# Optimization experiments

Measured on AMD Instinct MI355X. Metric: run time of the kernel, lower is better.

## Reference

```python
import jax, jax.numpy as jnp
from jax import lax
import numpy as np

B, T, U, V = 8, 256, 101, 512  # batch, max frames, max labels + 1, vocab (blank = 0)
BLANK = 0
NEG = -1e30  # finite -inf substitute (grad-safe in logaddexp)


def setup_inputs() -> dict:
    key = jax.random.key(0)
    k1, k2 = jax.random.split(key)
    acts = jax.random.normal(k1, (B, T, U, V), dtype=jnp.float32)
    labels = jax.random.randint(k2, (B, U - 1), 1, V).astype(jnp.int32)  # avoid blank idx
    act_lens = jnp.full((B,), T, dtype=jnp.int32)
    label_lens = jnp.full((B,), U - 1, dtype=jnp.int32)
    return {"acts": acts, "labels": labels, "act_lens": act_lens, "label_lens": label_lens}


def _rnnt_per_example(blankp, emit, tlen, ulen):
    # blankp: (T, U) log P(blank | t, u); emit: (T, U-1) log P(label_u | t, u)
    # alpha[0, u] = cumsum_u emit[0, :u]
    row0 = jnp.concatenate([jnp.zeros((1,), blankp.dtype), jnp.cumsum(emit[0])])

    # per-row recurrence: alpha[t, u] = logaddexp(alpha[t-1, u] + blank[t-1, u],
    #                                             alpha[t, u-1] + emit[t, u-1])
    # linear log-space recurrence x_u = logaddexp(b_u, x_{u-1} + a_u) -> associative scan
    def combine(l, r):
        aL, bL = l
        aR, bR = r
        return aL + aR, jnp.logaddexp(bR, bL + aR)

    def step(prev_row, xs):
        blank_tm1, emit_t = xs
        b = prev_row + blank_tm1                              # vertical (blank) transition
        a = jnp.concatenate([jnp.full((1,), NEG, blankp.dtype), emit_t])  # horizontal (emit)
        _, x = lax.associative_scan(combine, (a, b))
        return x, x

    _, rows = lax.scan(step, row0, (blankp[:-1], emit[1:]))
    alpha = jnp.concatenate([row0[None, :], rows], axis=0)    # (T, U)
    # loss = -log P(y|x) = -(alpha[T-1, U_label] + log P(blank | T-1, U_label))
    return -(alpha[tlen - 1, ulen] + blankp[tlen - 1, ulen])


def rnnt_loss(acts, labels, act_lens, label_lens):
    logp = jax.nn.log_softmax(acts, axis=-1)                  # (B, T, U, V)
    blankp = logp[..., BLANK]                                 # (B, T, U)
    lab = jnp.broadcast_to(
        labels[:, None, :, None].astype(jnp.int32),
        (acts.shape[0], acts.shape[1], labels.shape[1], 1),
    )
    emit = jnp.take_along_axis(logp[:, :, :-1, :], lab, axis=3)[..., 0]  # (B, T, U-1)
    return jax.vmap(_rnnt_per_example)(blankp, emit, act_lens, label_lens)


def reference(acts, labels, act_lens, label_lens):
    # reduction='none': per-example RNNT negative log-likelihood, shape (B,)
    return rnnt_loss(acts, labels, act_lens, label_lens)
```

## Files before the change

### kernel.cpp

```cpp
#include <hip/hip_runtime.h>

#define B_ 8
#define T_ 256
#define U_ 101
#define V_ 512
#define UM1 (U_ - 1)
#define DSTR 128
#define DALLOC 488
#define CH 32
#define NCH 12
#define CS 512.0f
#define LOG2E 1.4426950408889634f
#define LN2 0.6931471805599453f

typedef float floatx4 __attribute__((ext_vector_type(4)));
typedef float floatx2 __attribute__((ext_vector_type(2)));

__device__ __forceinline__ float wave_shr1_zero(float x) {
  int r = __builtin_amdgcn_update_dpp(0, __float_as_int(x), 0x138, 0xF, 0xF,
                                      false);
  return __int_as_float(r);
}

__global__ __launch_bounds__(256) void lse_kernel(
    const float* __restrict__ acts, const int* __restrict__ labels,
    const int* __restrict__ act_lens, const int* __restrict__ label_lens,
    float* __restrict__ blankD, float* __restrict__ emitD,
    float* __restrict__ bp2) {
  const int wv = blockIdx.x * 4 + (threadIdx.x >> 6);
  const int lane = threadIdx.x & 63;
  const int r0 = wv * 2;
  const int r1 = r0 + 1;
  const floatx4* p0 = (const floatx4*)(acts + (size_t)r0 * V_);
  const floatx4* p1 = (const floatx4*)(acts + (size_t)r1 * V_);
  floatx4 a0 = p0[lane];
  floatx4 a1 = p0[lane + 64];
  floatx4 c0 = p1[lane];
  floatx4 c1 = p1[lane + 64];
  float s0 = __builtin_exp2f(a0.x * LOG2E) + __builtin_exp2f(a0.y * LOG2E) +
             __builtin_exp2f(a0.z * LOG2E) + __builtin_exp2f(a0.w * LOG2E) +
             __builtin_exp2f(a1.x * LOG2E) + __builtin_exp2f(a1.y * LOG2E) +
             __builtin_exp2f(a1.z * LOG2E) + __builtin_exp2f(a1.w * LOG2E);
  float s1 = __builtin_exp2f(c0.x * LOG2E) + __builtin_exp2f(c0.y * LOG2E) +
             __builtin_exp2f(c0.z * LOG2E) + __builtin_exp2f(c0.w * LOG2E) +
             __builtin_exp2f(c1.x * LOG2E) + __builtin_exp2f(c1.y * LOG2E) +
             __builtin_exp2f(c1.z * LOG2E) + __builtin_exp2f(c1.w * LOG2E);
#pragma unroll
  for (int s = 32; s >= 1; s >>= 1) {
    s0 += __shfl_xor(s0, s);
    s1 += __shfl_xor(s1, s);
  }

#define EMIT_ROW(r, v0, v1, ssum)                                             \
  {                                                                           \
    const int u = (r) % U_;                                                   \
    const int bt = (r) / U_;                                                  \
    const int t = bt % T_;                                                    \
    const int b = bt / T_;                                                    \
    float emitv = 0.0f;                                                       \
    if (u < UM1) {                                                            \
      int e = labels[b * UM1 + u];                             \
      floatx4 sel = (e < 256) ? v0 : v1;                                      \
      int k = e & 3;                                                          \
      float cand =                                                            \
          (k == 0) ? sel.x : (k == 1) ? sel.y : (k == 2) ? sel.z : sel.w;     \
      emitv = __shfl(cand, (e & 255) >> 2);                                   \
    }                                                                         \
    if (lane == 0) {                                                          \
      const float rs = CS * __builtin_amdgcn_rcpf(ssum);                      \
      blankD[((size_t)b * DALLOC + (t + u + 1)) * DSTR + u] =                 \
          __builtin_exp2f(v0.x * LOG2E) * rs;                                 \
      if (u < UM1)                                                            \
        emitD[((size_t)b * DALLOC + (t + u + 1)) * DSTR + (u + 1)] =          \
            __builtin_exp2f(emitv * LOG2E) * rs;                              \
      if (t == act_lens[b] - 1 && u == label_lens[b])                         \
        bp2[b] = v0.x * LOG2E - __builtin_log2f(ssum);                        \
    }                                                                         \
  }

  EMIT_ROW(r0, a0, a1, s0)
  EMIT_ROW(r1, c0, c1, s1)
#undef EMIT_ROW
}

__global__ __launch_bounds__(64, 1) void dp_kernel(
    const float* __restrict__ blankD, const float* __restrict__ emitD,
    const float* __restrict__ bp2, const int* __restrict__ act_lens,
    const int* __restrict__ label_lens, float* __restrict__ out) {
  __shared__ float lds[2][2][CH][DSTR];
  const int b = blockIdx.x;
  const int lane = threadIdx.x;
  const int tl1 = act_lens[b] - 1;
  const int ulen = label_lens[b];
  const int dtar = tl1 + ulen;
  const bool capE = ((ulen & 1) == 0) && (lane == (ulen >> 1));
  const bool capO = ((ulen & 1) == 1) && (lane == (ulen >> 1));
  const floatx4* g4B = (const floatx4*)(blankD + (size_t)b * DALLOC * DSTR);
  const floatx4* g4E = (const floatx4*)(emitD + (size_t)b * DALLOC * DSTR);

  floatx4 rB[16], rE[16];
#pragma unroll
  for (int j = 0; j < 16; ++j) {
    rB[j] = g4B[32 + j * 64 + lane];
    rE[j] = g4E[32 + j * 64 + lane];
  }
  {
    floatx4* lB4 = (floatx4*)&lds[0][0][0][0];
    floatx4* lE4 = (floatx4*)&lds[0][1][0][0];
#pragma unroll
    for (int j = 0; j < 16; ++j) {
      lB4[j * 64 + lane] = rB[j];
      lE4[j * 64 + lane] = rE[j];
    }
  }
  float xE = (lane == 0) ? 1.0f : 0.0f;
  float xO = 0.0f;
  float res = 0.0f, capS = 0.0f, S = 0.0f;

  for (int c = 0; c < NCH; ++c) {
    const int buf = c & 1;
    const int nb = ((c + 1) * CH + 1) * 32;
#pragma unroll
    for (int j = 0; j < 16; ++j) {
      rB[j] = g4B[(size_t)nb + j * 64 + lane];
      rE[j] = g4E[(size_t)nb + j * 64 + lane];
    }
    const floatx2* lB2 = (const floatx2*)&lds[buf][0][0][0];
    const floatx2* lE2 = (const floatx2*)&lds[buf][1][0][0];
    floatx2 pB[8], pE[8];
#pragma unroll
    for (int k = 0; k < 8; ++k) {
      pB[k] = lB2[k * 64 + lane];
      pE[k] = lE2[k * 64 + lane];
    }
    const int dbase = c * CH + 1;
#pragma unroll
    for (int k = 0; k < CH; ++k) {
      const int d = dbase + k;
      const floatx2 Bv = pB[k & 7];
      const floatx2 Ev = pE[k & 7];
      if (k + 8 < CH) {
        pB[k & 7] = lB2[(k + 8) * 64 + lane];
        pE[k & 7] = lE2[(k + 8) * 64 + lane];
      }
      const float xm1E = wave_shr1_zero(xO);
      const float nxE = __builtin_fmaf(xE, Bv.x, xm1E * Ev.x);
      const float nxO = __builtin_fmaf(xO, Bv.y, xE * Ev.y);
      if (d == dtar) {
        res = capE ? nxE : (capO ? nxO : res);
        capS = S;
      }
      xE = nxE;
      xO = nxO;
    }
    float m = fmaxf(xE, xO);
#pragma unroll
    for (int s = 32; s >= 1; s >>= 1) m = fmaxf(m, __shfl_xor(m, s));
    if (m > 0.0f) {
      const float ex = floorf(__builtin_log2f(m));
      const float sc = __builtin_exp2f(-ex);
      xE *= sc;
      xO *= sc;
      S += ex;
    }
    floatx4* wB4 = (floatx4*)&lds[buf ^ 1][0][0][0];
    floatx4* wE4 = (floatx4*)&lds[buf ^ 1][1][0][0];
#pragma unroll
    for (int j = 0; j < 16; ++j) {
      wB4[j * 64 + lane] = rB[j];
      wE4[j * 64 + lane] = rE[j];
    }
  }
  if (capE || capO)
    out[b] = -((__builtin_log2f(res) + capS - 9.0f * (float)dtar + bp2[b]) *
               LN2);
}

extern "C" void kernel_launch(void* const* d_in, const int* in_sizes, int n_in,
                              void* d_out, int out_size, void* d_ws, size_t ws_size,
                              hipStream_t stream) {
  const float* acts = (const float*)d_in[0];
  const int* labels = (const int*)d_in[1];
  const int* act_lens = (const int*)d_in[2];
  const int* label_lens = (const int*)d_in[3];
  float* out = (float*)d_out;
  float* blankD = (float*)d_ws;
  float* emitD = blankD + (size_t)B_ * DALLOC * DSTR;
  float* bp2 = emitD + (size_t)B_ * DALLOC * DSTR;
  hipMemsetAsync(blankD, 0, (size_t)2 * B_ * DALLOC * DSTR * sizeof(float),
                 stream);
  const int nwaves2 = B_ * T_ * U_ / 2;
  lse_kernel<<<nwaves2 / 4, 256, 0, stream>>>(acts, labels, act_lens,
                                              label_lens, blankD, emitD, bp2);
  dp_kernel<<<B_, 64, 0, stream>>>(blankD, emitD, bp2, act_lens, label_lens,
                                   out);
}
```

Measured before the change: 103.6 us.

## Split RNNT DP into forward and backward halves meeting at mid-diagonal

The serial anti-diagonal recurrence per batch is split into a forward pass from the start and a backward (beta) pass from the end, each covering about half the diagonals on separate workgroups (16 blocks instead of 8). A small combine kernel takes the dot product of the two state vectors at the meeting diagonal to get the total probability. This halves the serial dependency chain of the latency-bound DP. In exchange it adds a kernel launch and relies on the backward transitions and scaling bookkeeping being correct for general lengths.

Result: faster. 95.57 us (-7.7%).

```diff
diff --git a/kernel.cpp b/kernel.cpp
--- a/kernel.cpp
+++ b/kernel.cpp
@@ -8,7 +8,7 @@
 #define DSTR 128
 #define DALLOC 488
 #define CH 32
-#define NCH 12
+#define NCHD 6
 #define CS 512.0f
 #define LOG2E 1.4426950408889634f
 #define LN2 0.6931471805599453f
@@ -21,12 +21,15 @@
                                       false);
   return __int_as_float(r);
 }
+__device__ __forceinline__ float wave_shl1_zero(float x) {
+  int r = __builtin_amdgcn_update_dpp(0, __float_as_int(x), 0x130, 0xF, 0xF,
+                                      false);
+  return __int_as_float(r);
+}
 
 __global__ __launch_bounds__(256) void lse_kernel(
     const float* __restrict__ acts, const int* __restrict__ labels,
-    const int* __restrict__ act_lens, const int* __restrict__ label_lens,
-    float* __restrict__ blankD, float* __restrict__ emitD,
-    float* __restrict__ bp2) {
+    float* __restrict__ blankD, float* __restrict__ emitD) {
   const int wv = blockIdx.x * 4 + (threadIdx.x >> 6);
   const int lane = threadIdx.x & 63;
   const int r0 = wv * 2;
@@ -73,8 +76,6 @@
       if (u < UM1)                                                            \
         emitD[((size_t)b * DALLOC + (t + u + 1)) * DSTR + (u + 1)] =          \
             __builtin_exp2f(emitv * LOG2E) * rs;                              \
-      if (t == act_lens[b] - 1 && u == label_lens[b])                         \
-        bp2[b] = v0.x * LOG2E - __builtin_log2f(ssum);                        \
     }                                                                         \
   }
 
@@ -85,95 +86,188 @@
 
 __global__ __launch_bounds__(64, 1) void dp_kernel(
     const float* __restrict__ blankD, const float* __restrict__ emitD,
-    const float* __restrict__ bp2, const int* __restrict__ act_lens,
-    const int* __restrict__ label_lens, float* __restrict__ out) {
+    const int* __restrict__ act_lens, const int* __restrict__ label_lens,
+    float* __restrict__ stateA, float* __restrict__ stateB) {
   __shared__ float lds[2][2][CH][DSTR];
-  const int b = blockIdx.x;
+  const int bid = blockIdx.x;
+  const int b = bid & 7;
+  const bool fwd = (bid < 8);
   const int lane = threadIdx.x;
   const int tl1 = act_lens[b] - 1;
   const int ulen = label_lens[b];
   const int dtar = tl1 + ulen;
-  const bool capE = ((ulen & 1) == 0) && (lane == (ulen >> 1));
-  const bool capO = ((ulen & 1) == 1) && (lane == (ulen >> 1));
+  const int dmid = dtar >> 1;
   const floatx4* g4B = (const floatx4*)(blankD + (size_t)b * DALLOC * DSTR);
   const floatx4* g4E = (const floatx4*)(emitD + (size_t)b * DALLOC * DSTR);
-
   floatx4 rB[16], rE[16];
-#pragma unroll
-  for (int j = 0; j < 16; ++j) {
-    rB[j] = g4B[32 + j * 64 + lane];
-    rE[j] = g4E[32 + j * 64 + lane];
-  }
-  {
-    floatx4* lB4 = (floatx4*)&lds[0][0][0][0];
-    floatx4* lE4 = (floatx4*)&lds[0][1][0][0];
+  float xE, xO, S = 0.0f;
+
+  if (fwd) {
 #pragma unroll
     for (int j = 0; j < 16; ++j) {
-      lB4[j * 64 + lane] = rB[j];
-      lE4[j * 64 + lane] = rE[j];
-    }
-  }
-  float xE = (lane == 0) ? 1.0f : 0.0f;
-  float xO = 0.0f;
-  float res = 0.0f, capS = 0.0f, S = 0.0f;
-
-  for (int c = 0; c < NCH; ++c) {
-    const int buf = c & 1;
-    const int nb = ((c + 1) * CH + 1) * 32;
+      rB[j] = g4B[32 + j * 64 + lane];
+      rE[j] = g4E[32 + j * 64 + lane];
+    }
+    {
+      floatx4* lB4 = (floatx4*)&lds[0][0][0][0];
+      floatx4* lE4 = (floatx4*)&lds[0][1][0][0];
+#pragma unroll
+      for (int j = 0; j < 16; ++j) {
+        lB4[j * 64 + lane] = rB[j];
+        lE4[j * 64 + lane] = rE[j];
+      }
+    }
+    xE = (lane == 0) ? 1.0f : 0.0f;
+    xO = 0.0f;
+    for (int c = 0; c < NCHD; ++c) {
+      const int buf = c & 1;
+      const int nb = ((c + 1) * CH + 1) * 32;
+#pragma unroll
+      for (int j = 0; j < 16; ++j) {
+        rB[j] = g4B[(size_t)nb + j * 64 + lane];
+        rE[j] = g4E[(size_t)nb + j * 64 + lane];
+      }
+      const floatx2* lB2 = (const floatx2*)&lds[buf][0][0][0];
+      const floatx2* lE2 = (const floatx2*)&lds[buf][1][0][0];
+      floatx2 pB[8], pE[8];
+#pragma unroll
+      for (int k = 0; k < 8; ++k) {
+        pB[k] = lB2[k * 64 + lane];
+        pE[k] = lE2[k * 64 + lane];
+      }
+      const int dbase = c * CH + 1;
+#pragma unroll
+      for (int k = 0; k < CH; ++k) {
+        const int d = dbase + k;
+        const floatx2 Bv = pB[k & 7];
+        const floatx2 Ev = pE[k & 7];
+        if (k + 8 < CH) {
+          pB[k & 7] = lB2[(k + 8) * 64 + lane];
+          pE[k & 7] = lE2[(k + 8) * 64 + lane];
+        }
+        const float xm1E = wave_shr1_zero(xO);
+        const float nxE = __builtin_fmaf(xE, Bv.x, xm1E * Ev.x);
+        const float nxO = __builtin_fmaf(xO, Bv.y, xE * Ev.y);
+        const bool go = (d <= dmid);
+        xE = go ? nxE : xE;
+        xO = go ? nxO : xO;
+      }
+      float m = fmaxf(xE, xO);
+#pragma unroll
+      for (int s = 32; s >= 1; s >>= 1) m = fmaxf(m, __shfl_xor(m, s));
+      if (m > 0.0f) {
+        const float ex = floorf(__builtin_log2f(m));
+        const float sc = __builtin_exp2f(-ex);
+        xE *= sc;
+        xO *= sc;
+        S += ex;
+      }
+      floatx4* wB4 = (floatx4*)&lds[buf ^ 1][0][0][0];
+      floatx4* wE4 = (floatx4*)&lds[buf ^ 1][1][0][0];
+#pragma unroll
+      for (int j = 0; j < 16; ++j) {
+        wB4[j * 64 + lane] = rB[j];
+        wE4[j * 64 + lane] = rE[j];
+      }
+    }
+    float* sA = stateA + b * 132;
+    ((floatx2*)sA)[lane] = floatx2{xE, xO};
+    if (lane == 0) sA[128] = S;
+  } else {
+    const int R00 = dtar - 31;
 #pragma unroll
     for (int j = 0; j < 16; ++j) {
-      rB[j] = g4B[(size_t)nb + j * 64 + lane];
-      rE[j] = g4E[(size_t)nb + j * 64 + lane];
-    }
-    const floatx2* lB2 = (const floatx2*)&lds[buf][0][0][0];
-    const floatx2* lE2 = (const floatx2*)&lds[buf][1][0][0];
-    floatx2 pB[8], pE[8];
-#pragma unroll
-    for (int k = 0; k < 8; ++k) {
-      pB[k] = lB2[k * 64 + lane];
-      pE[k] = lE2[k * 64 + lane];
-    }
-    const int dbase = c * CH + 1;
-#pragma unroll
-    for (int k = 0; k < CH; ++k) {
-      const int d = dbase + k;
-      const floatx2 Bv = pB[k & 7];
-      const floatx2 Ev = pE[k & 7];
-      if (k + 8 < CH) {
-        pB[k & 7] = lB2[(k + 8) * 64 + lane];
-        pE[k & 7] = lE2[(k + 8) * 64 + lane];
-      }
-      const float xm1E = wave_shr1_zero(xO);
-      const float nxE = __builtin_fmaf(xE, Bv.x, xm1E * Ev.x);
-      const float nxO = __builtin_fmaf(xO, Bv.y, xE * Ev.y);
-      if (d == dtar) {
-        res = capE ? nxE : (capO ? nxO : res);
-        capS = S;
-      }
-      xE = nxE;
-      xO = nxO;
-    }
-    float m = fmaxf(xE, xO);
-#pragma unroll
-    for (int s = 32; s >= 1; s >>= 1) m = fmaxf(m, __shfl_xor(m, s));
-    if (m > 0.0f) {
-      const float ex = floorf(__builtin_log2f(m));
-      const float sc = __builtin_exp2f(-ex);
-      xE *= sc;
-      xO *= sc;
-      S += ex;
-    }
-    floatx4* wB4 = (floatx4*)&lds[buf ^ 1][0][0][0];
-    floatx4* wE4 = (floatx4*)&lds[buf ^ 1][1][0][0];
-#pragma unroll
-    for (int j = 0; j < 16; ++j) {
-      wB4[j * 64 + lane] = rB[j];
-      wE4[j * 64 + lane] = rE[j];
-    }
-  }
-  if (capE || capO)
-    out[b] = -((__builtin_log2f(res) + capS - 9.0f * (float)dtar + bp2[b]) *
+      rB[j] = g4B[(size_t)R00 * 32 + j * 64 + lane];
+      rE[j] = g4E[(size_t)R00 * 32 + j * 64 + lane];
+    }
+    {
+      floatx4* lB4 = (floatx4*)&lds[0][0][0][0];
+      floatx4* lE4 = (floatx4*)&lds[0][1][0][0];
+#pragma unroll
+      for (int j = 0; j < 16; ++j) {
+        lB4[j * 64 + lane] = rB[j];
+        lE4[j * 64 + lane] = rE[j];
+      }
+    }
+    const float seed = blankD[((size_t)b * DALLOC + dtar + 1) * DSTR + ulen];
+    xE = (lane == (ulen >> 1) && !(ulen & 1)) ? seed : 0.0f;
+    xO = (lane == (ulen >> 1) && (ulen & 1)) ? seed : 0.0f;
+    const int smax = dtar - 1 - dmid;
+    for (int c = 0; c < NCHD; ++c) {
+      const int buf = c & 1;
+      const int R0n = max(R00 - 32 * (c + 1), 0);
+#pragma unroll
+      for (int j = 0; j < 16; ++j) {
+        rB[j] = g4B[(size_t)R0n * 32 + j * 64 + lane];
+        rE[j] = g4E[(size_t)R0n * 32 + j * 64 + lane];
+      }
+      const floatx2* lB2 = (const floatx2*)&lds[buf][0][0][0];
+      const floatx2* lE2 = (const floatx2*)&lds[buf][1][0][0];
+      floatx2 pB[8], pE[8];
+#pragma unroll
+      for (int k = 0; k < 8; ++k) {
+        pB[k] = lB2[(31 - k) * 64 + lane];
+        pE[k] = lE2[(31 - k) * 64 + lane];
+      }
+#pragma unroll
+      for (int k = 0; k < CH; ++k) {
+        const int s = c * CH + k;
+        const floatx2 Bv = pB[k & 7];
+        const floatx2 Ev = pE[k & 7];
+        if (k + 8 < CH) {
+          pB[k & 7] = lB2[(31 - (k + 8)) * 64 + lane];
+          pE[k & 7] = lE2[(31 - (k + 8)) * 64 + lane];
+        }
+        const float tO = wave_shl1_zero(Ev.x * xE);
+        const float nxE = __builtin_fmaf(xE, Bv.x, Ev.y * xO);
+        const float nxO = __builtin_fmaf(xO, Bv.y, tO);
+        const bool go = (s <= smax);
+        xE = go ? nxE : xE;
+        xO = go ? nxO : xO;
+      }
+      float m = fmaxf(xE, xO);
+#pragma unroll
+      for (int s2 = 32; s2 >= 1; s2 >>= 1) m = fmaxf(m, __shfl_xor(m, s2));
+      if (m > 0.0f) {
+        const float ex = floorf(__builtin_log2f(m));
+        const float sc = __builtin_exp2f(-ex);
+        xE *= sc;
+        xO *= sc;
+        S += ex;
+      }
+      floatx4* wB4 = (floatx4*)&lds[buf ^ 1][0][0][0];
+      floatx4* wE4 = (floatx4*)&lds[buf ^ 1][1][0][0];
+#pragma unroll
+      for (int j = 0; j < 16; ++j) {
+        wB4[j * 64 + lane] = rB[j];
+        wE4[j * 64 + lane] = rE[j];
+      }
+    }
+    float* sB = stateB + b * 132;
+    ((floatx2*)sB)[lane] = floatx2{xE, xO};
+    if (lane == 0) sB[128] = S;
+  }
+}
+
+__global__ __launch_bounds__(64) void combine_kernel(
+    const float* __restrict__ stateA, const float* __restrict__ stateB,
+    const int* __restrict__ act_lens, const int* __restrict__ label_lens,
+    float* __restrict__ out) {
+  const int b = blockIdx.x;
+  const int lane = threadIdx.x;
+  const float* sA = stateA + b * 132;
+  const float* sB = stateB + b * 132;
+  const floatx2 a = ((const floatx2*)sA)[lane];
+  const floatx2 bb = ((const floatx2*)sB)[lane];
+  float p = a.x * bb.x + a.y * bb.y;
+#pragma unroll
+  for (int s = 32; s >= 1; s >>= 1) p += __shfl_xor(p, s);
+  if (lane == 0) {
+    const int dtar = act_lens[b] - 1 + label_lens[b];
+    out[b] = -((__builtin_log2f(p) + sA[128] + sB[128] -
+                9.0f * (float)(dtar + 1)) *
                LN2);
+  }
 }
 
 extern "C" void kernel_launch(void* const* d_in, const int* in_sizes, int n_in,
@@ -186,12 +280,14 @@
   float* out = (float*)d_out;
   float* blankD = (float*)d_ws;
   float* emitD = blankD + (size_t)B_ * DALLOC * DSTR;
-  float* bp2 = emitD + (size_t)B_ * DALLOC * DSTR;
+  float* stateA = emitD + (size_t)B_ * DALLOC * DSTR;
+  float* stateB = stateA + B_ * 132;
   hipMemsetAsync(blankD, 0, (size_t)2 * B_ * DALLOC * DSTR * sizeof(float),
                  stream);
   const int nwaves2 = B_ * T_ * U_ / 2;
-  lse_kernel<<<nwaves2 / 4, 256, 0, stream>>>(acts, labels, act_lens,
-                                              label_lens, blankD, emitD, bp2);
-  dp_kernel<<<B_, 64, 0, stream>>>(blankD, emitD, bp2, act_lens, label_lens,
-                                   out);
-}
+  lse_kernel<<<nwaves2 / 4, 256, 0, stream>>>(acts, labels, blankD, emitD);
+  dp_kernel<<<16, 64, 0, stream>>>(blankD, emitD, act_lens, label_lens,
+                                   stateA, stateB);
+  combine_kernel<<<B_, 64, 0, stream>>>(stateA, stateB, act_lens, label_lens,
+                                        out);
+}
```
